# Kernel tuning notes

Hardware: AMD Instinct MI355X
Metric: run time of the kernel (lower is better)

## Reference

```python
import jax, jax.numpy as jnp
import numpy as np

N_HID = 4096   # n_hidden_states (rows of M_h / M_p)
N_TH = 4096    # n_token_H (hidden state width, GRU hidden size)
N_TP = 4096    # n_token_P (GRU input size)
N_LABEL = 3
K_STEPS = 8


def setup_inputs() -> dict:
    key = jax.random.key(0)
    ks = jax.random.split(key, 7)
    maxL = max(N_TH, N_TP)
    return {
        "M_h": jax.random.normal(ks[0], (N_HID, N_TH), jnp.float32),
        "M_p": jax.random.normal(ks[1], (N_HID, N_TP), jnp.float32),
        "w1": jax.random.normal(ks[2], (N_HID, 1), jnp.float32) * 0.05,
        "W2": jax.random.normal(ks[3], (N_HID, N_TH), jnp.float32) * 0.02,
        "W3": jax.random.normal(ks[4], (N_TH + N_TP + 2 * maxL, N_LABEL), jnp.float32) * 0.02,
        "gru_w_ih": jax.random.normal(ks[5], (3 * N_TH, N_TP), jnp.float32) * 0.02,
        "gru_w_hh": jax.random.normal(ks[6], (3 * N_TH, N_TH), jnp.float32) * 0.02,
        "K": K_STEPS,
    }


def _gru_cell(x, h, w_ih, w_hh):
    # torch.nn.GRUCell with bias=False; x:(1,n_in), h:(1,n_hid)
    gi = x @ w_ih.T                      # (1, 3*n_hid)
    gh = h @ w_hh.T                      # (1, 3*n_hid)
    i_r, i_z, i_n = jnp.split(gi, 3, axis=1)
    h_r, h_z, h_n = jnp.split(gh, 3, axis=1)
    r = jax.nn.sigmoid(i_r + h_r)
    z = jax.nn.sigmoid(i_z + h_z)
    n = jnp.tanh(i_n + r * h_n)
    return (1.0 - z) * n + z * h


def reference(M_h, M_p, w1, W2, W3, gru_w_ih, gru_w_hh, K):
    n_rows = M_h.shape[0]                 # n_hidden_states
    nH, nP = M_h.shape[1], M_p.shape[1]
    maxL = max(nH, nP)
    n_label = W3.shape[1]

    # alpha = softmax(w1^T M_h); __compute_k_th only uses first n_rows coeffs
    alpha = jax.nn.softmax(w1.T @ M_h, axis=1)          # (1, nH)
    sk0 = alpha[:, :n_rows] @ M_h                       # (1, nH)

    # W2^T @ M_p is loop-invariant -> hoist the big GEMM
    C = W2.T @ M_p                                      # (nH, nP)

    def step(carry, _):
        sk, P_r = carry
        beta = jax.nn.softmax(sk @ C, axis=1)           # (1, nP)
        xk = beta[:, :n_rows] @ M_p                     # (1, nP)
        sk_new = _gru_cell(xk, sk, gru_w_ih, gru_w_hh)  # (1, nH)
        sk1 = jnp.pad(sk_new, ((0, 0), (0, maxL - nH)))
        xk1 = jnp.pad(xk, ((0, 0), (0, maxL - nP)))
        feat = jnp.concatenate(
            [sk_new, xk, jnp.abs(sk1 - xk1), sk1 * xk1], axis=1
        ).T                                             # (nH+nP+2*maxL, 1)
        P_r = P_r + jax.nn.softmax(W3.T @ feat, axis=0) # (n_label, 1)
        return (sk_new, P_r), None

    P_r0 = jnp.zeros((n_label, 1), dtype=M_h.dtype)
    (_, P_r), _ = jax.lax.scan(step, (sk0, P_r0), None, length=K)
    return P_r.T / K
```

## Files before the change

kernel.cpp:

```cpp
#include <hip/hip_runtime.h>
#include <hip/hip_bf16.h>
#include <math.h>

#define N      4096
#define KSTEPS 8
#define NF     16384

__global__ void colsum_kernel(const float* __restrict__ M,
                              const float* __restrict__ w,
                              float* __restrict__ out,
                              int rowsPerSlice) {
    int c4 = blockIdx.x * blockDim.x + threadIdx.x;
    int i0 = blockIdx.y * rowsPerSlice;
    float4 acc = make_float4(0.f, 0.f, 0.f, 0.f);
    for (int i = i0; i < i0 + rowsPerSlice; ++i) {
        float wi = w[i];
        float4 m = ((const float4*)(M + (size_t)i * N))[c4];
        acc.x += wi * m.x;
        acc.y += wi * m.y;
        acc.z += wi * m.z;
        acc.w += wi * m.w;
    }
    atomicAdd(&out[c4 * 4 + 0], acc.x);
    atomicAdd(&out[c4 * 4 + 1], acc.y);
    atomicAdd(&out[c4 * 4 + 2], acc.z);
    atomicAdd(&out[c4 * 4 + 3], acc.w);
}

__global__ void rowdot_u_kernel(const float* __restrict__ W2,
                                const float* __restrict__ sk,
                                float* __restrict__ u,
                                float* __restrict__ bufv) {
    int row = blockIdx.x;
    const float4* r = (const float4*)(W2 + (size_t)row * N);
    const float4* x = (const float4*)sk;
    float acc = 0.f;
    for (int c = threadIdx.x; c < N / 4; c += blockDim.x) {
        float4 a = r[c];
        float4 b = x[c];
        acc += a.x * b.x + a.y * b.y + a.z * b.z + a.w * b.w;
    }
    __shared__ float red[256];
    red[threadIdx.x] = acc;
    __syncthreads();
    for (int s = 128; s > 0; s >>= 1) {
        if (threadIdx.x < s) red[threadIdx.x] += red[threadIdx.x + s];
        __syncthreads();
    }
    if (threadIdx.x == 0) {
        u[row]    = red[0];
        bufv[row] = 0.f;
    }
}

__global__ void softmax_kernel(const float* __restrict__ v,
                               float* __restrict__ wgt,
                               float* __restrict__ zbuf) {
    __shared__ float red[1024];
    int tid = threadIdx.x;
    float m = -1e30f;
    for (int i = tid; i < N; i += 1024) m = fmaxf(m, v[i]);
    red[tid] = m;
    __syncthreads();
    for (int s = 512; s > 0; s >>= 1) {
        if (tid < s) red[tid] = fmaxf(red[tid], red[tid + s]);
        __syncthreads();
    }
    float mx = red[0];
    __syncthreads();
    float sum = 0.f;
    for (int i = tid; i < N; i += 1024) {
        float e = expf(v[i] - mx);
        wgt[i] = e;
        sum += e;
    }
    red[tid] = sum;
    __syncthreads();
    for (int s = 512; s > 0; s >>= 1) {
        if (tid < s) red[tid] += red[tid + s];
        __syncthreads();
    }
    float inv = 1.f / red[0];
    for (int i = tid; i < N; i += 1024) wgt[i] *= inv;
    if (zbuf) {
        for (int i = tid; i < N; i += 1024) zbuf[i] = 0.f;
    }
}

__global__ void gru_kernel(const float* __restrict__ w_ih,
                           const float* __restrict__ w_hh,
                           const float* __restrict__ xk,
                           const float* __restrict__ h,
                           float* __restrict__ h_out,
                           float* __restrict__ logits3) {
    int t = blockIdx.x;
    float acc[6] = {0.f, 0.f, 0.f, 0.f, 0.f, 0.f};
    const float4* xv = (const float4*)xk;
    const float4* hv = (const float4*)h;
    for (int g = 0; g < 3; ++g) {
        const float4* wi = (const float4*)(w_ih + (size_t)(g * N + t) * N);
        const float4* wh = (const float4*)(w_hh + (size_t)(g * N + t) * N);
        for (int c = threadIdx.x; c < N / 4; c += blockDim.x) {
            float4 a = wi[c], b = xv[c];
            acc[g] += a.x * b.x + a.y * b.y + a.z * b.z + a.w * b.w;
            float4 a2 = wh[c], b2 = hv[c];
            acc[3 + g] += a2.x * b2.x + a2.y * b2.y + a2.z * b2.z + a2.w * b2.w;
        }
    }
    __shared__ float red[6][256];
    for (int g = 0; g < 6; ++g) red[g][threadIdx.x] = acc[g];
    __syncthreads();
    for (int s = 128; s > 0; s >>= 1) {
        if (threadIdx.x < s)
            for (int g = 0; g < 6; ++g)
                red[g][threadIdx.x] += red[g][threadIdx.x + s];
        __syncthreads();
    }
    if (threadIdx.x == 0) {
        float ir = red[0][0], iz = red[1][0], in_ = red[2][0];
        float hr = red[3][0], hz = red[4][0], hn = red[5][0];
        float r = 1.f / (1.f + expf(-(ir + hr)));
        float z = 1.f / (1.f + expf(-(iz + hz)));
        float n = tanhf(in_ + r * hn);
        h_out[t] = (1.f - z) * n + z * h[t];
        if (t < 3) logits3[t] = 0.f;
    }
}

__global__ void feat_kernel(const float* __restrict__ W3,
                            const float* __restrict__ s,
                            const float* __restrict__ x,
                            float* __restrict__ logits3) {
    int f = blockIdx.x * blockDim.x + threadIdx.x;
    int j = f & (N - 1);
    int seg = f >> 12;
    float sv = s[j], xv = x[j];
    float val;
    if (seg == 0)      val = sv;
    else if (seg == 1) val = xv;
    else if (seg == 2) val = fabsf(sv - xv);
    else               val = sv * xv;
    float l0 = val * W3[f * 3 + 0];
    float l1 = val * W3[f * 3 + 1];
    float l2 = val * W3[f * 3 + 2];

    __shared__ float red[3][256];
    red[0][threadIdx.x] = l0;
    red[1][threadIdx.x] = l1;
    red[2][threadIdx.x] = l2;
    __syncthreads();
    for (int st = 128; st > 0; st >>= 1) {
        if (threadIdx.x < st)
            for (int g = 0; g < 3; ++g)
                red[g][threadIdx.x] += red[g][threadIdx.x + st];
        __syncthreads();
    }
    if (threadIdx.x == 0) {
        atomicAdd(&logits3[0], red[0][0]);
        atomicAdd(&logits3[1], red[1][0]);
        atomicAdd(&logits3[2], red[2][0]);
    }
}

__global__ void acc3_kernel(const float* __restrict__ l3,
                            float* __restrict__ Pr,
                            float* __restrict__ out,
                            int finalize) {
    if (threadIdx.x == 0 && blockIdx.x == 0) {
        float a = l3[0], b = l3[1], c = l3[2];
        float m = fmaxf(a, fmaxf(b, c));
        float e0 = expf(a - m), e1 = expf(b - m), e2 = expf(c - m);
        float s = e0 + e1 + e2;
        float p0 = Pr[0] + e0 / s;
        float p1 = Pr[1] + e1 / s;
        float p2 = Pr[2] + e2 / s;
        Pr[0] = p0; Pr[1] = p1; Pr[2] = p2;
        if (finalize) {
            out[0] = p0 / (float)KSTEPS;
            out[1] = p1 / (float)KSTEPS;
            out[2] = p2 / (float)KSTEPS;
        }
    }
}

extern "C" void kernel_launch(void* const* d_in, const int* in_sizes, int n_in,
                              void* d_out, int out_size, void* d_ws, size_t ws_size,
                              hipStream_t stream) {
    const float* M_h  = (const float*)d_in[0];
    const float* M_p  = (const float*)d_in[1];
    const float* w1   = (const float*)d_in[2];
    const float* W2   = (const float*)d_in[3];
    const float* W3   = (const float*)d_in[4];
    const float* w_ih = (const float*)d_in[5];
    const float* w_hh = (const float*)d_in[6];
    float* out = (float*)d_out;

    float* ws    = (float*)d_ws;
    float* buf_v = ws;
    float* buf_w = ws + 4096;
    float* sk_a  = ws + 8192;
    float* sk_b  = ws + 12288;
    float* xk    = ws + 16384;
    float* u     = ws + 20480;
    float* l3    = ws + 24576;
    float* Pr    = ws + 24579;

    hipMemsetAsync(d_ws, 0, (size_t)24592 * sizeof(float), stream);

    dim3 csGrid(4, 128);

    colsum_kernel<<<csGrid, 256, 0, stream>>>(M_h, w1, buf_v, 32);
    softmax_kernel<<<1, 1024, 0, stream>>>(buf_v, buf_w, nullptr);
    colsum_kernel<<<csGrid, 256, 0, stream>>>(M_h, buf_w, sk_a, 32);

    float* h  = sk_a;
    float* hn = sk_b;
    for (int k = 0; k < KSTEPS; ++k) {
        rowdot_u_kernel<<<4096, 256, 0, stream>>>(W2, h, u, buf_v);
        colsum_kernel<<<csGrid, 256, 0, stream>>>(M_p, u, buf_v, 32);
        softmax_kernel<<<1, 1024, 0, stream>>>(buf_v, buf_w, xk);
        colsum_kernel<<<csGrid, 256, 0, stream>>>(M_p, buf_w, xk, 32);
        gru_kernel<<<4096, 256, 0, stream>>>(w_ih, w_hh, xk, h, hn, l3);
        feat_kernel<<<64, 256, 0, stream>>>(W3, hn, xk, l3);
        acc3_kernel<<<1, 64, 0, stream>>>(l3, Pr, out, k == KSTEPS - 1 ? 1 : 0);
        float* t = h; h = hn; hn = t;
    }
}
```

Measured before the change: 1.612 ms.

## Convert large weight matrices to fp16 once and stream halves in the recurrent loop

Adds conversion kernels that turn W2, M_p, and the GRU input and hidden weights into fp16 copies in the workspace at the start of each call. The per-step matvec and column-sum kernels then read these half-precision copies and accumulate in fp32, halving the bytes streamed across the eight recurrent steps. It also merges the feature-logit reduction and the 3-way softmax accumulation into one single-block kernel, dropping a launch and the atomics. The conversion pass reads all fp32 weights once per call, and the fp16 storage lowers precision relative to the fp32 reference.

```diff
diff --git a/kernel.cpp b/kernel.cpp
--- a/kernel.cpp
+++ b/kernel.cpp
@@ -1,10 +1,25 @@
 #include <hip/hip_runtime.h>
 #include <hip/hip_bf16.h>
+#include <hip/hip_fp16.h>
 #include <math.h>
 
 #define N      4096
 #define KSTEPS 8
 #define NF     16384
+
+__global__ void cvt_kernel(const float* __restrict__ src,
+                           __half* __restrict__ dst) {
+    size_t idx = (size_t)blockIdx.x * blockDim.x + threadIdx.x;
+    const float4* s4 = (const float4*)src;
+    float4 a = s4[2 * idx];
+    float4 b = s4[2 * idx + 1];
+    union { float4 f; __half2 h[4]; } u;
+    u.h[0] = __floats2half2_rn(a.x, a.y);
+    u.h[1] = __floats2half2_rn(a.z, a.w);
+    u.h[2] = __floats2half2_rn(b.x, b.y);
+    u.h[3] = __floats2half2_rn(b.z, b.w);
+    ((float4*)dst)[idx] = u.f;
+}
 
 __global__ void colsum_kernel(const float* __restrict__ M,
                               const float* __restrict__ w,
@@ -27,18 +42,49 @@
     atomicAdd(&out[c4 * 4 + 3], acc.w);
 }
 
-__global__ void rowdot_u_kernel(const float* __restrict__ W2,
+__global__ void colsum_h_kernel(const __half* __restrict__ M,
+                                const float* __restrict__ w,
+                                float* __restrict__ out,
+                                int rowsPerSlice) {
+    int c8 = blockIdx.x * blockDim.x + threadIdx.x;
+    int i0 = blockIdx.y * rowsPerSlice;
+    float acc[8] = {0.f, 0.f, 0.f, 0.f, 0.f, 0.f, 0.f, 0.f};
+    for (int i = i0; i < i0 + rowsPerSlice; ++i) {
+        float wi = w[i];
+        union { float4 f; __half2 h[4]; } u;
+        u.f = ((const float4*)(M + (size_t)i * N))[c8];
+        float2 p0 = __half22float2(u.h[0]);
+        float2 p1 = __half22float2(u.h[1]);
+        float2 p2 = __half22float2(u.h[2]);
+        float2 p3 = __half22float2(u.h[3]);
+        acc[0] += wi * p0.x; acc[1] += wi * p0.y;
+        acc[2] += wi * p1.x; acc[3] += wi * p1.y;
+        acc[4] += wi * p2.x; acc[5] += wi * p2.y;
+        acc[6] += wi * p3.x; acc[7] += wi * p3.y;
+    }
+    int base = c8 * 8;
+    #pragma unroll
+    for (int q = 0; q < 8; ++q) atomicAdd(&out[base + q], acc[q]);
+}
+
+__global__ void rowdot_h_kernel(const __half* __restrict__ W2h,
                                 const float* __restrict__ sk,
                                 float* __restrict__ u,
                                 float* __restrict__ bufv) {
     int row = blockIdx.x;
-    const float4* r = (const float4*)(W2 + (size_t)row * N);
+    const float4* r = (const float4*)(W2h + (size_t)row * N);
     const float4* x = (const float4*)sk;
     float acc = 0.f;
-    for (int c = threadIdx.x; c < N / 4; c += blockDim.x) {
-        float4 a = r[c];
-        float4 b = x[c];
-        acc += a.x * b.x + a.y * b.y + a.z * b.z + a.w * b.w;
+    for (int c = threadIdx.x; c < N / 8; c += blockDim.x) {
+        union { float4 f; __half2 h[4]; } w;
+        w.f = r[c];
+        float4 x0 = x[2 * c], x1 = x[2 * c + 1];
+        float2 p0 = __half22float2(w.h[0]);
+        float2 p1 = __half22float2(w.h[1]);
+        float2 p2 = __half22float2(w.h[2]);
+        float2 p3 = __half22float2(w.h[3]);
+        acc += p0.x * x0.x + p0.y * x0.y + p1.x * x0.z + p1.y * x0.w
+             + p2.x * x1.x + p2.y * x1.y + p3.x * x1.z + p3.y * x1.w;
     }
     __shared__ float red[256];
     red[threadIdx.x] = acc;
@@ -87,12 +133,11 @@
     }
 }
 
-__global__ void gru_kernel(const float* __restrict__ w_ih,
-                           const float* __restrict__ w_hh,
-                           const float* __restrict__ xk,
-                           const float* __restrict__ h,
-                           float* __restrict__ h_out,
-                           float* __restrict__ logits3) {
+__global__ void gru_h_kernel(const __half* __restrict__ w_ih,
+                             const __half* __restrict__ w_hh,
+                             const float* __restrict__ xk,
+                             const float* __restrict__ h,
+                             float* __restrict__ h_out) {
     int t = blockIdx.x;
     float acc[6] = {0.f, 0.f, 0.f, 0.f, 0.f, 0.f};
     const float4* xv = (const float4*)xk;
@@ -100,11 +145,20 @@
     for (int g = 0; g < 3; ++g) {
         const float4* wi = (const float4*)(w_ih + (size_t)(g * N + t) * N);
         const float4* wh = (const float4*)(w_hh + (size_t)(g * N + t) * N);
-        for (int c = threadIdx.x; c < N / 4; c += blockDim.x) {
-            float4 a = wi[c], b = xv[c];
-            acc[g] += a.x * b.x + a.y * b.y + a.z * b.z + a.w * b.w;
-            float4 a2 = wh[c], b2 = hv[c];
-            acc[3 + g] += a2.x * b2.x + a2.y * b2.y + a2.z * b2.z + a2.w * b2.w;
+        for (int c = threadIdx.x; c < N / 8; c += blockDim.x) {
+            union { float4 f; __half2 h2[4]; } a, b;
+            a.f = wi[c];
+            b.f = wh[c];
+            float4 x0 = xv[2 * c], x1 = xv[2 * c + 1];
+            float4 h0 = hv[2 * c], h1 = hv[2 * c + 1];
+            float2 a0 = __half22float2(a.h2[0]), a1 = __half22float2(a.h2[1]);
+            float2 a2 = __half22float2(a.h2[2]), a3 = __half22float2(a.h2[3]);
+            float2 b0 = __half22float2(b.h2[0]), b1 = __half22float2(b.h2[1]);
+            float2 b2 = __half22float2(b.h2[2]), b3 = __half22float2(b.h2[3]);
+            acc[g]     += a0.x * x0.x + a0.y * x0.y + a1.x * x0.z + a1.y * x0.w
+                        + a2.x * x1.x + a2.y * x1.y + a3.x * x1.z + a3.y * x1.w;
+            acc[3 + g] += b0.x * h0.x + b0.y * h0.y + b1.x * h0.z + b1.y * h0.w
+                        + b2.x * h1.x + b2.y * h1.y + b3.x * h1.z + b3.y * h1.w;
         }
     }
     __shared__ float red[6][256];
@@ -123,57 +177,49 @@
         float z = 1.f / (1.f + expf(-(iz + hz)));
         float n = tanhf(in_ + r * hn);
         h_out[t] = (1.f - z) * n + z * h[t];
-        if (t < 3) logits3[t] = 0.f;
-    }
-}
-
-__global__ void feat_kernel(const float* __restrict__ W3,
-                            const float* __restrict__ s,
-                            const float* __restrict__ x,
-                            float* __restrict__ logits3) {
-    int f = blockIdx.x * blockDim.x + threadIdx.x;
-    int j = f & (N - 1);
-    int seg = f >> 12;
-    float sv = s[j], xv = x[j];
-    float val;
-    if (seg == 0)      val = sv;
-    else if (seg == 1) val = xv;
-    else if (seg == 2) val = fabsf(sv - xv);
-    else               val = sv * xv;
-    float l0 = val * W3[f * 3 + 0];
-    float l1 = val * W3[f * 3 + 1];
-    float l2 = val * W3[f * 3 + 2];
-
-    __shared__ float red[3][256];
-    red[0][threadIdx.x] = l0;
-    red[1][threadIdx.x] = l1;
-    red[2][threadIdx.x] = l2;
-    __syncthreads();
-    for (int st = 128; st > 0; st >>= 1) {
-        if (threadIdx.x < st)
-            for (int g = 0; g < 3; ++g)
-                red[g][threadIdx.x] += red[g][threadIdx.x + st];
-        __syncthreads();
-    }
-    if (threadIdx.x == 0) {
-        atomicAdd(&logits3[0], red[0][0]);
-        atomicAdd(&logits3[1], red[1][0]);
-        atomicAdd(&logits3[2], red[2][0]);
-    }
-}
-
-__global__ void acc3_kernel(const float* __restrict__ l3,
-                            float* __restrict__ Pr,
-                            float* __restrict__ out,
-                            int finalize) {
-    if (threadIdx.x == 0 && blockIdx.x == 0) {
-        float a = l3[0], b = l3[1], c = l3[2];
-        float m = fmaxf(a, fmaxf(b, c));
-        float e0 = expf(a - m), e1 = expf(b - m), e2 = expf(c - m);
-        float s = e0 + e1 + e2;
-        float p0 = Pr[0] + e0 / s;
-        float p1 = Pr[1] + e1 / s;
-        float p2 = Pr[2] + e2 / s;
+    }
+}
+
+__global__ void feat3_kernel(const float* __restrict__ W3,
+                             const float* __restrict__ s,
+                             const float* __restrict__ x,
+                             float* __restrict__ Pr,
+                             float* __restrict__ out,
+                             int finalize) {
+    __shared__ float red[3][1024];
+    int tid = threadIdx.x;
+    float a0 = 0.f, a1 = 0.f, a2 = 0.f;
+    for (int f = tid; f < NF; f += 1024) {
+        int j = f & (N - 1);
+        int seg = f >> 12;
+        float sv = s[j], xv = x[j];
+        float val;
+        if (seg == 0)      val = sv;
+        else if (seg == 1) val = xv;
+        else if (seg == 2) val = fabsf(sv - xv);
+        else               val = sv * xv;
+        a0 += val * W3[f * 3 + 0];
+        a1 += val * W3[f * 3 + 1];
+        a2 += val * W3[f * 3 + 2];
+    }
+    red[0][tid] = a0; red[1][tid] = a1; red[2][tid] = a2;
+    __syncthreads();
+    for (int st = 512; st > 0; st >>= 1) {
+        if (tid < st) {
+            red[0][tid] += red[0][tid + st];
+            red[1][tid] += red[1][tid + st];
+            red[2][tid] += red[2][tid + st];
+        }
+        __syncthreads();
+    }
+    if (tid == 0) {
+        float la = red[0][0], lb = red[1][0], lc = red[2][0];
+        float m = fmaxf(la, fmaxf(lb, lc));
+        float e0 = expf(la - m), e1 = expf(lb - m), e2 = expf(lc - m);
+        float ssum = e0 + e1 + e2;
+        float p0 = Pr[0] + e0 / ssum;
+        float p1 = Pr[1] + e1 / ssum;
+        float p2 = Pr[2] + e2 / ssum;
         Pr[0] = p0; Pr[1] = p1; Pr[2] = p2;
         if (finalize) {
             out[0] = p0 / (float)KSTEPS;
@@ -195,34 +241,45 @@
     const float* w_hh = (const float*)d_in[6];
     float* out = (float*)d_out;
 
-    float* ws    = (float*)d_ws;
-    float* buf_v = ws;
-    float* buf_w = ws + 4096;
-    float* sk_a  = ws + 8192;
-    float* sk_b  = ws + 12288;
-    float* xk    = ws + 16384;
-    float* u     = ws + 20480;
-    float* l3    = ws + 24576;
-    float* Pr    = ws + 24579;
-
-    hipMemsetAsync(d_ws, 0, (size_t)24592 * sizeof(float), stream);
-
-    dim3 csGrid(4, 128);
-
-    colsum_kernel<<<csGrid, 256, 0, stream>>>(M_h, w1, buf_v, 32);
+    char* base = (char*)d_ws;
+    const size_t SZ_NN  = (size_t)N * N * sizeof(__half);
+    const size_t SZ_3NN = (size_t)3 * N * N * sizeof(__half);
+    __half* W2h  = (__half*)(base);
+    __half* M_ph = (__half*)(base + SZ_NN);
+    __half* wihh = (__half*)(base + 2 * SZ_NN);
+    __half* whhh = (__half*)(base + 2 * SZ_NN + SZ_3NN);
+    float*  fs   = (float*)(base + 2 * SZ_NN + 2 * SZ_3NN);
+    float* buf_v = fs;
+    float* buf_w = fs + 4096;
+    float* sk_a  = fs + 8192;
+    float* sk_b  = fs + 12288;
+    float* xk    = fs + 16384;
+    float* u     = fs + 20480;
+    float* Pr    = fs + 24576;
+
+    hipMemsetAsync(fs, 0, (size_t)24580 * sizeof(float), stream);
+
+    cvt_kernel<<<(N / 8) * (N / 256), 256, 0, stream>>>(W2,   W2h);
+    cvt_kernel<<<(N / 8) * (N / 256), 256, 0, stream>>>(M_p,  M_ph);
+    cvt_kernel<<<3 * (N / 8) * (N / 256), 256, 0, stream>>>(w_ih, wihh);
+    cvt_kernel<<<3 * (N / 8) * (N / 256), 256, 0, stream>>>(w_hh, whhh);
+
+    dim3 cs32(4, 128);
+    colsum_kernel<<<cs32, 256, 0, stream>>>(M_h, w1, buf_v, 32);
     softmax_kernel<<<1, 1024, 0, stream>>>(buf_v, buf_w, nullptr);
-    colsum_kernel<<<csGrid, 256, 0, stream>>>(M_h, buf_w, sk_a, 32);
-
+    colsum_kernel<<<cs32, 256, 0, stream>>>(M_h, buf_w, sk_a, 32);
+
+    dim3 cs16(2, 128);
     float* h  = sk_a;
     float* hn = sk_b;
     for (int k = 0; k < KSTEPS; ++k) {
-        rowdot_u_kernel<<<4096, 256, 0, stream>>>(W2, h, u, buf_v);
-        colsum_kernel<<<csGrid, 256, 0, stream>>>(M_p, u, buf_v, 32);
+        rowdot_h_kernel<<<4096, 256, 0, stream>>>(W2h, h, u, buf_v);
+        colsum_h_kernel<<<cs16, 256, 0, stream>>>(M_ph, u, buf_v, 32);
         softmax_kernel<<<1, 1024, 0, stream>>>(buf_v, buf_w, xk);
-        colsum_kernel<<<csGrid, 256, 0, stream>>>(M_p, buf_w, xk, 32);
-        gru_kernel<<<4096, 256, 0, stream>>>(w_ih, w_hh, xk, h, hn, l3);
-        feat_kernel<<<64, 256, 0, stream>>>(W3, hn, xk, l3);
-        acc3_kernel<<<1, 64, 0, stream>>>(l3, Pr, out, k == KSTEPS - 1 ? 1 : 0);
+        colsum_h_kernel<<<cs16, 256, 0, stream>>>(M_ph, buf_w, xk, 32);
+        gru_h_kernel<<<4096, 256, 0, stream>>>(wihh, whhh, xk, h, hn);
+        feat3_kernel<<<1, 1024, 0, stream>>>(W3, hn, xk, Pr, out,
+                                             k == KSTEPS - 1 ? 1 : 0);
         float* t = h; h = hn; hn = t;
     }
 }
```

Result: slower. 1.653 ms (+2.5%).
